# Optimization experiments

Measured on AMD Instinct MI355X. Metric: run time of the kernel, lower is better.

The kernel has to match this reference:

```python
import jax, jax.numpy as jnp
import numpy as np

N_NODES = 50000
N_EDGES = 800000
NODE_DIM = 128
EDGE_DIM = 16
HIDDEN = 64


def _gcn_conv(x, W, b, src, dst, n_nodes):
    """PyG-style GCNConv: add self-loops, symmetric deg^-1/2 normalization,
    aggregate messages from src into dst, then add bias. x: [N, Fin]."""
    h = x @ W  # [N, Fout]
    loops = jnp.arange(n_nodes)
    s = jnp.concatenate([src, loops])  # sources incl. self-loops
    d = jnp.concatenate([dst, loops])  # targets incl. self-loops
    deg = jax.ops.segment_sum(jnp.ones_like(d, dtype=h.dtype), d, num_segments=n_nodes)
    dinv = jax.lax.rsqrt(jnp.maximum(deg, 1.0))  # deg >= 1 thanks to self-loops
    norm = dinv[s] * dinv[d]  # [E+N]
    msg = h[s] * norm[:, None]  # gather + scale
    out = jax.ops.segment_sum(msg, d, num_segments=n_nodes)  # scatter-add
    return out + b


def setup_inputs() -> dict:
    key = jax.random.key(0)
    ks = jax.random.split(key, 12)
    x = jax.random.normal(ks[0], (N_NODES, NODE_DIM), dtype=jnp.float32)
    edge_index = jax.random.randint(ks[1], (2, N_EDGES), 0, N_NODES, dtype=jnp.int64)
    edge_attr = jax.random.normal(ks[2], (N_EDGES, EDGE_DIM), dtype=jnp.float32)
    def glorot(k, fan_in, fan_out):
        s = float(np.sqrt(2.0 / (fan_in + fan_out)))
        return jax.random.normal(k, (fan_in, fan_out), dtype=jnp.float32) * s
    W1 = glorot(ks[3], NODE_DIM, HIDDEN)
    b1 = jnp.zeros((HIDDEN,), jnp.float32)
    W2 = glorot(ks[4], HIDDEN, HIDDEN)
    b2 = jnp.zeros((HIDDEN,), jnp.float32)
    Wm1 = glorot(ks[5], 2 * HIDDEN + EDGE_DIM, HIDDEN)
    bm1 = jnp.zeros((HIDDEN,), jnp.float32)
    Wm2 = glorot(ks[6], HIDDEN, 2)
    bm2 = jnp.zeros((2,), jnp.float32)
    return {"x": x, "edge_index": edge_index, "edge_attr": edge_attr,
            "W1": W1, "b1": b1, "W2": W2, "b2": b2,
            "Wm1": Wm1, "bm1": bm1, "Wm2": Wm2, "bm2": bm2}


def reference(x, edge_index, edge_attr, W1, b1, W2, b2, Wm1, bm1, Wm2, bm2):
    n = x.shape[0]
    src, dst = edge_index[0], edge_index[1]
    h = jax.nn.relu(_gcn_conv(x, W1, b1, src, dst, n))
    h = jax.nn.relu(_gcn_conv(h, W2, b2, src, dst, n))
    # gather endpoint embeddings + concat edge features -> edge MLP
    edge_embed = jnp.concatenate([h[src], h[dst], edge_attr], axis=1)  # [E, 2H+Fe]
    out = jax.nn.relu(edge_embed @ Wm1 + bm1) @ Wm2 + bm2  # [E, 2]
    return out
```

## Files before the change

### kernel.cpp

```cpp
#include <hip/hip_runtime.h>
#include <hip/hip_fp16.h>


typedef float v4f __attribute__((ext_vector_type(4)));
typedef _Float16 v4h __attribute__((ext_vector_type(4)));

__device__ __forceinline__ float4 relu4(float4 v) {
    v.x = fmaxf(v.x, 0.f); v.y = fmaxf(v.y, 0.f);
    v.z = fmaxf(v.z, 0.f); v.w = fmaxf(v.w, 0.f);
    return v;
}

__device__ __forceinline__ void load_lds16(const void* g, void* l) {
    __builtin_amdgcn_global_load_lds(
        (const __attribute__((address_space(1))) void*)g,
        (__attribute__((address_space(3))) void*)l, 16, 0, 0);
}

__global__ void k_count(const int* __restrict__ dst, int* __restrict__ cnt,
                        int* __restrict__ rank, int E) {
    int e = blockIdx.x * 256 + threadIdx.x;
    if (e < E) rank[e] = atomicAdd(&cnt[dst[e]], 1);
}

__global__ void k_bsum(const int* __restrict__ cnt, int* __restrict__ bsum,
                       float* __restrict__ dinv, int N) {
    int i = blockIdx.x * 256 + threadIdx.x;
    int v = (i < N) ? cnt[i] : 0;
    if (i < N) dinv[i] = rsqrtf((float)v + 1.0f);
    int r = v;
#pragma unroll
    for (int d = 1; d < 64; d <<= 1) r += __shfl_xor(r, d);
    __shared__ int ws[4];
    if ((threadIdx.x & 63) == 0) ws[threadIdx.x >> 6] = r;
    __syncthreads();
    if (threadIdx.x == 0) bsum[blockIdx.x] = ws[0] + ws[1] + ws[2] + ws[3];
}

__global__ void k_scanb(int* __restrict__ bsum, int nb) {
    int t = threadIdx.x;
    int lane = t & 63, w = t >> 6;
    int v = (t < nb) ? bsum[t] : 0;
    int x = v;
#pragma unroll
    for (int d = 1; d < 64; d <<= 1) {
        int y = __shfl_up(x, d);
        if (lane >= d) x += y;
    }
    __shared__ int ws[4];
    if (lane == 63) ws[w] = x;
    __syncthreads();
    int woff = 0;
    for (int j = 0; j < w; j++) woff += ws[j];
    if (t < nb) bsum[t] = woff + x - v;
}

__global__ void k_scan3(const int* __restrict__ cnt, const int* __restrict__ bsum,
                        int* __restrict__ row_ptr, int N, int E) {
    int t = threadIdx.x, b = blockIdx.x;
    int i = b * 256 + t;
    int lane = t & 63, w = t >> 6;
    int v = (i < N) ? cnt[i] : 0;
    int x = v;
#pragma unroll
    for (int d = 1; d < 64; d <<= 1) {
        int y = __shfl_up(x, d);
        if (lane >= d) x += y;
    }
    __shared__ int ws[4];
    if (lane == 63) ws[w] = x;
    __syncthreads();
    int woff = 0;
    for (int j = 0; j < w; j++) woff += ws[j];
    if (i < N) row_ptr[i] = bsum[b] + woff + x - v;
    if (i == 0) row_ptr[N] = E;
}

__global__ void k_fill(const int* __restrict__ src, const int* __restrict__ dst,
                       const int* __restrict__ row_ptr, const int* __restrict__ rank,
                       int* __restrict__ csr_src, int E) {
    int e = blockIdx.x * 256 + threadIdx.x;
    if (e >= E) return;
    csr_src[row_ptr[dst[e]] + rank[e]] = src[e];
}

template<int K, bool RELU_A, bool SCALE, int NB>
__global__ __launch_bounds__(256) void k_mgemm(
    const float* __restrict__ A, const float* __restrict__ B0,
    const float* __restrict__ B1, const float* __restrict__ bias,
    const float* __restrict__ dinv, __half* __restrict__ C0,
    __half* __restrict__ C1, int M) {
    constexpr int P = K + 8;
    __shared__ __half As[64 * P];
    __shared__ __half Bs[NB * 64 * P];
    const int t = threadIdx.x;
    const int r0 = blockIdx.x * 64;

    constexpr int C4 = K / 4;
    for (int idx = t; idx < 64 * C4; idx += 256) {
        int row = idx / C4, c4 = idx % C4;
        float4 v = make_float4(0.f, 0.f, 0.f, 0.f);
        if (r0 + row < M)
            v = reinterpret_cast<const float4*>(A + (size_t)(r0 + row) * K)[c4];
        if (RELU_A) v = relu4(v);
        __half* d = &As[row * P + 4 * c4];
        d[0] = __float2half(v.x); d[1] = __float2half(v.y);
        d[2] = __float2half(v.z); d[3] = __float2half(v.w);
    }
    for (int m = 0; m < NB; m++) {
        const float* Bm = m ? B1 : B0;
        __half* Bsm = &Bs[m * 64 * P];
        for (int idx = t; idx < K * 16; idx += 256) {
            int k = idx >> 4, c4 = idx & 15;
            float4 v = reinterpret_cast<const float4*>(Bm + (size_t)k * 64)[c4];
            Bsm[(4 * c4 + 0) * P + k] = __float2half(v.x);
            Bsm[(4 * c4 + 1) * P + k] = __float2half(v.y);
            Bsm[(4 * c4 + 2) * P + k] = __float2half(v.z);
            Bsm[(4 * c4 + 3) * P + k] = __float2half(v.w);
        }
    }
    __syncthreads();

    const int lane = t & 63, w = t >> 6;
    const int li = lane & 15, g = lane >> 4;

    v4f acc[NB][4];
    const v4f zero = {0.f, 0.f, 0.f, 0.f};
#pragma unroll
    for (int m = 0; m < NB; m++)
#pragma unroll
        for (int c = 0; c < 4; c++) acc[m][c] = zero;

#pragma unroll
    for (int kk = 0; kk < K; kk += 16) {
        v4h a = *reinterpret_cast<const v4h*>(&As[(16 * w + li) * P + kk + 4 * g]);
#pragma unroll
        for (int m = 0; m < NB; m++) {
#pragma unroll
            for (int c = 0; c < 4; c++) {
                v4h b = *reinterpret_cast<const v4h*>(
                    &Bs[m * 64 * P + (16 * c + li) * P + kk + 4 * g]);
                acc[m][c] =
                    __builtin_amdgcn_mfma_f32_16x16x16f16(a, b, acc[m][c], 0, 0, 0);
            }
        }
    }

    const int rbase = r0 + 16 * w + 4 * g;
    float4 dv = make_float4(1.f, 1.f, 1.f, 1.f);
    if (SCALE) dv = *reinterpret_cast<const float4*>(&dinv[rbase]);
    const float sc[4] = {dv.x, dv.y, dv.z, dv.w};
#pragma unroll
    for (int m = 0; m < NB; m++) {
        __half* C = m ? C1 : C0;
#pragma unroll
        for (int c = 0; c < 4; c++) {
            int col = 16 * c + li;
            float badd = (NB == 2 && m == 0) ? bias[col] : 0.f;
#pragma unroll
            for (int r = 0; r < 4; r++) {
                int gr = rbase + r;
                if (gr < M)
                    C[(size_t)gr * 64 + col] =
                        __float2half(acc[m][c][r] * sc[r] + badd);
            }
        }
    }
}

__global__ __launch_bounds__(256, 4) void k_agg(const __half* __restrict__ A16,
                                                const int* __restrict__ row_ptr,
                                                const int* __restrict__ csr_src,
                                                const float* __restrict__ dinv,
                                                const float* __restrict__ bias,
                                                float* __restrict__ out, int N) {
    int gw = (blockIdx.x * 256 + threadIdx.x) >> 6;
    int sub = (threadIdx.x >> 4) & 3;
    int l = threadIdx.x & 15;
    int node = gw * 4 + sub;
    if (node >= N) return;
    const uint2* A4 = reinterpret_cast<const uint2*>(A16);

    int beg = row_ptr[node], end = row_ptr[node + 1];
    uint2 selfv = A4[(size_t)node * 16 + l];
    float2 a0 = __half22float2(*reinterpret_cast<__half2*>(&selfv.x));
    float2 a1 = __half22float2(*reinterpret_cast<__half2*>(&selfv.y));
    float4 acc = make_float4(a0.x, a0.y, a1.x, a1.y);

#define ACC(u)                                                          \
    {                                                                   \
        float2 f0 = __half22float2(*reinterpret_cast<__half2*>(&u.x));  \
        float2 f1 = __half22float2(*reinterpret_cast<__half2*>(&u.y));  \
        acc.x += f0.x; acc.y += f0.y; acc.z += f1.x; acc.w += f1.y;     \
    }
    for (int p = beg; p < end; p += 16) {
        int m = min(16, end - p);
        int sl = (p + l < end) ? csr_src[p + l] : 0;
        int j = 0;
        for (; j + 7 < m; j += 8) {
            uint2 u0 = A4[(size_t)__shfl(sl, j + 0, 16) * 16 + l];
            uint2 u1 = A4[(size_t)__shfl(sl, j + 1, 16) * 16 + l];
            uint2 u2 = A4[(size_t)__shfl(sl, j + 2, 16) * 16 + l];
            uint2 u3 = A4[(size_t)__shfl(sl, j + 3, 16) * 16 + l];
            uint2 u4 = A4[(size_t)__shfl(sl, j + 4, 16) * 16 + l];
            uint2 u5 = A4[(size_t)__shfl(sl, j + 5, 16) * 16 + l];
            uint2 u6 = A4[(size_t)__shfl(sl, j + 6, 16) * 16 + l];
            uint2 u7 = A4[(size_t)__shfl(sl, j + 7, 16) * 16 + l];
            ACC(u0) ACC(u1) ACC(u2) ACC(u3) ACC(u4) ACC(u5) ACC(u6) ACC(u7)
        }
        for (; j + 3 < m; j += 4) {
            uint2 u0 = A4[(size_t)__shfl(sl, j + 0, 16) * 16 + l];
            uint2 u1 = A4[(size_t)__shfl(sl, j + 1, 16) * 16 + l];
            uint2 u2 = A4[(size_t)__shfl(sl, j + 2, 16) * 16 + l];
            uint2 u3 = A4[(size_t)__shfl(sl, j + 3, 16) * 16 + l];
            ACC(u0) ACC(u1) ACC(u2) ACC(u3)
        }
        for (; j < m; j++) {
            uint2 u0 = A4[(size_t)__shfl(sl, j, 16) * 16 + l];
            ACC(u0)
        }
    }
#undef ACC
    float di = dinv[node];
    float4 bb = *reinterpret_cast<const float4*>(&bias[4 * l]);
    float4 o = make_float4(fmaf(di, acc.x, bb.x), fmaf(di, acc.y, bb.y),
                           fmaf(di, acc.z, bb.z), fmaf(di, acc.w, bb.w));
    *reinterpret_cast<float4*>(&out[(size_t)node * 64 + 4 * l]) = o;
}

__global__ __launch_bounds__(256, 4) void k_edge(
    const __half* __restrict__ Ps, const __half* __restrict__ Pd,
    const int* __restrict__ src, const int* __restrict__ dst,
    const float* __restrict__ ea, const float* __restrict__ We,
    const float* __restrict__ Wm2, const float* __restrict__ bm2,
    float* __restrict__ out, int E) {
    __shared__ __align__(16) char smem[4 * 12288];
    const int lane = threadIdx.x & 63;
    const int wid = (blockIdx.x * 256 + threadIdx.x) >> 6;
    const int li = lane & 15, g = lane >> 4;
    const int e0 = wid * 64;
    if (e0 >= E) return;

    char* wbase = smem + (threadIdx.x >> 6) * 12288;
    const float4* ea4 = reinterpret_cast<const float4*>(ea);

    v4h af[4];
#pragma unroll
    for (int m = 0; m < 4; m++) {
        v4h a;
#pragma unroll
        for (int i = 0; i < 4; i++)
            a[i] = (_Float16)We[(4 * g + i) * 64 + 16 * m + li];
        af[m] = a;
    }

    float4 w2lo[4], w2hi[4];
#pragma unroll
    for (int m = 0; m < 4; m++) {
        int dim0 = 16 * m + 4 * g;
        w2lo[m] = *reinterpret_cast<const float4*>(&Wm2[2 * dim0]);
        w2hi[m] = *reinterpret_cast<const float4*>(&Wm2[2 * dim0 + 4]);
    }
    const float c0 = bm2[0], c1 = bm2[1];

    const int ecl = min(e0 + lane, E - 1);
    const int sv = src[ecl], dv = dst[ecl];

    v4h bh[4];
#pragma unroll
    for (int n = 0; n < 4; n++) {
        int ee = min(e0 + 16 * n + li, E - 1);
        float4 bf = ea4[(size_t)ee * 4 + g];
        v4h t;
        t[0] = (_Float16)bf.x; t[1] = (_Float16)bf.y;
        t[2] = (_Float16)bf.z; t[3] = (_Float16)bf.w;
        bh[n] = t;
    }

    const int jrow = lane >> 3;
    const int csw = (lane & 7) ^ jrow;

#define STAGE(n, b)                                                              \
    {                                                                            \
        char* lb = wbase + (b) * 4096 + lane * 16;                               \
        int n0 = __shfl(sv, 16 * (n) + jrow);                                    \
        int n1 = __shfl(sv, 16 * (n) + 8 + jrow);                                \
        int n2 = __shfl(dv, 16 * (n) + jrow);                                    \
        int n3 = __shfl(dv, 16 * (n) + 8 + jrow);                                \
        load_lds16((const char*)Ps + (size_t)n0 * 128 + (csw << 4), lb);         \
        load_lds16((const char*)Ps + (size_t)n1 * 128 + (csw << 4), lb + 1024);  \
        load_lds16((const char*)Pd + (size_t)n2 * 128 + (csw << 4), lb + 2048);  \
        load_lds16((const char*)Pd + (size_t)n3 * 128 + (csw << 4), lb + 3072);  \
    }

    float p0s[4], p1s[4];

#define COMPUTE(n, b)                                                             \
    {                                                                             \
        const char* rb = wbase + (b) * 4096;                                      \
        uint2 us[4], ud[4];                                                       \
        _Pragma("unroll")                                                         \
        for (int m = 0; m < 4; m++) {                                             \
            int q = 4 * m + g;                                                    \
            int off = li * 128 + ((((q >> 1) ^ (li & 7)) << 4) | ((q & 1) << 3)); \
            us[m] = *reinterpret_cast<const uint2*>(rb + off);                    \
            ud[m] = *reinterpret_cast<const uint2*>(rb + 2048 + off);             \
        }                                                                         \
        float p0_ = 0.f, p1_ = 0.f;                                               \
        _Pragma("unroll")                                                         \
        for (int m = 0; m < 4; m++) {                                             \
            float2 s0 = __half22float2(*reinterpret_cast<__half2*>(&us[m].x));    \
            float2 s1 = __half22float2(*reinterpret_cast<__half2*>(&us[m].y));    \
            float2 d0 = __half22float2(*reinterpret_cast<__half2*>(&ud[m].x));    \
            float2 d1 = __half22float2(*reinterpret_cast<__half2*>(&ud[m].y));    \
            v4f c;                                                                \
            c[0] = s0.x + d0.x;                                                   \
            c[1] = s0.y + d0.y;                                                   \
            c[2] = s1.x + d1.x;                                                   \
            c[3] = s1.y + d1.y;                                                   \
            v4f q = __builtin_amdgcn_mfma_f32_16x16x16f16(af[m], bh[n], c, 0, 0, 0); \
            float u0 = fmaxf(q[0], 0.f), u1 = fmaxf(q[1], 0.f);                   \
            float u2 = fmaxf(q[2], 0.f), u3 = fmaxf(q[3], 0.f);                   \
            p0_ += u0 * w2lo[m].x + u1 * w2lo[m].z + u2 * w2hi[m].x + u3 * w2hi[m].z; \
            p1_ += u0 * w2lo[m].y + u1 * w2lo[m].w + u2 * w2hi[m].y + u3 * w2hi[m].w; \
        }                                                                         \
        p0_ += __shfl_xor(p0_, 16); p0_ += __shfl_xor(p0_, 32);                   \
        p1_ += __shfl_xor(p1_, 16); p1_ += __shfl_xor(p1_, 32);                   \
        p0s[n] = p0_; p1s[n] = p1_;                                               \
    }

    STAGE(0, 0)
    STAGE(1, 1)
    STAGE(2, 2)
    asm volatile("s_waitcnt vmcnt(8)" ::: "memory");
    COMPUTE(0, 0)
    STAGE(3, 0)
    asm volatile("s_waitcnt vmcnt(8)" ::: "memory");
    COMPUTE(1, 1)
    asm volatile("s_waitcnt vmcnt(4)" ::: "memory");
    COMPUTE(2, 2)
    asm volatile("s_waitcnt vmcnt(0)" ::: "memory");
    COMPUTE(3, 0)
#undef STAGE
#undef COMPUTE

    if (g == 0) {
#pragma unroll
        for (int n = 0; n < 4; n++) {
            int e = e0 + 16 * n + li;
            if (e < E)
                *reinterpret_cast<float2*>(&out[(size_t)e * 2]) =
                    make_float2(p0s[n] + c0, p1s[n] + c1);
        }
    }
}

static inline size_t align256(size_t x) { return (x + 255) & ~(size_t)255; }

extern "C" void kernel_launch(void* const* d_in, const int* in_sizes, int n_in,
                              void* d_out, int out_size, void* d_ws, size_t ws_size,
                              hipStream_t stream) {
    const float* x = (const float*)d_in[0];
    const int* ei = (const int*)d_in[1];
    const float* ea = (const float*)d_in[2];
    const float* W1 = (const float*)d_in[3];
    const float* b1 = (const float*)d_in[4];
    const float* W2 = (const float*)d_in[5];
    const float* b2 = (const float*)d_in[6];
    const float* Wm1 = (const float*)d_in[7];
    const float* bm1 = (const float*)d_in[8];
    const float* Wm2 = (const float*)d_in[9];
    const float* bm2 = (const float*)d_in[10];

    const int N = in_sizes[0] / 128;
    const int E = in_sizes[1] / 2;
    const int* src = ei;
    const int* dst = ei + E;
    float* out = (float*)d_out;

    const int NB = (N + 255) / 256;

    char* p = (char*)d_ws;
    int* cnt = (int*)p;        p += align256((size_t)N * 4);
    int* rank = (int*)p;       p += align256((size_t)E * 4);
    int* row_ptr = (int*)p;    p += align256((size_t)(N + 1) * 4);
    int* bsum = (int*)p;       p += align256((size_t)NB * 4);
    int* csr_src = (int*)p;    p += align256((size_t)E * 4);
    float* dinv = (float*)p;   p += align256((size_t)N * 4);
    __half* A16 = (__half*)p;  p += align256((size_t)N * 64 * 2);
    float* B = (float*)p;      p += align256((size_t)N * 64 * 4);
    __half* Ps16 = (__half*)p; p += align256((size_t)N * 64 * 2);
    __half* Pd16 = (__half*)p;

    hipMemsetAsync(cnt, 0, (size_t)N * sizeof(int), stream);
    k_count<<<(E + 255) / 256, 256, 0, stream>>>(dst, cnt, rank, E);
    k_bsum<<<NB, 256, 0, stream>>>(cnt, bsum, dinv, N);
    k_scanb<<<1, 256, 0, stream>>>(bsum, NB);
    k_scan3<<<NB, 256, 0, stream>>>(cnt, bsum, row_ptr, N, E);
    k_fill<<<(E + 255) / 256, 256, 0, stream>>>(src, dst, row_ptr, rank, csr_src, E);

    const int GB = (N + 63) / 64;

    k_mgemm<128, false, true, 1><<<GB, 256, 0, stream>>>(
        x, W1, nullptr, nullptr, dinv, A16, nullptr, N);
    k_agg<<<(N + 15) / 16, 256, 0, stream>>>(A16, row_ptr, csr_src, dinv, b1, B, N);

    k_mgemm<64, true, true, 1><<<GB, 256, 0, stream>>>(
        B, W2, nullptr, nullptr, dinv, A16, nullptr, N);
    k_agg<<<(N + 15) / 16, 256, 0, stream>>>(A16, row_ptr, csr_src, dinv, b2, B, N);

    k_mgemm<64, true, false, 2><<<GB, 256, 0, stream>>>(
        B, Wm1, Wm1 + 64 * 64, bm1, nullptr, Ps16, Pd16, N);
    int waves = (E + 63) / 64;
    k_edge<<<(waves + 3) / 4, 256, 0, stream>>>(Ps16, Pd16, src, dst, ea,
                                                Wm1 + 128 * 64, Wm2, bm2,
                                                out, E);
}
```

Before: 276.4 us.

## Fuse neighbor aggregation with the following GEMM via shared-memory tiles

Merges each GCN aggregation kernel with the next dense matmul. The aggregated, ReLU'd rows are written as fp16 into shared memory and fed directly to MFMA instead of going through a float32 global buffer. This removes the fp32 intermediate round trip and two kernel launches. In exchange, each block now runs the irregular gather before its GEMM, and occupancy is no longer governed by the separate launch bounds, so latency hiding for the gathers may change.

```diff
diff --git a/kernel.cpp b/kernel.cpp
--- a/kernel.cpp
+++ b/kernel.cpp
@@ -84,15 +84,13 @@
     csr_src[row_ptr[dst[e]] + rank[e]] = src[e];
 }
 
-template<int K, bool RELU_A, bool SCALE, int NB>
+template<int K, bool RELU_A, bool SCALE>
 __global__ __launch_bounds__(256) void k_mgemm(
     const float* __restrict__ A, const float* __restrict__ B0,
-    const float* __restrict__ B1, const float* __restrict__ bias,
-    const float* __restrict__ dinv, __half* __restrict__ C0,
-    __half* __restrict__ C1, int M) {
+    const float* __restrict__ dinv, __half* __restrict__ C0, int M) {
     constexpr int P = K + 8;
     __shared__ __half As[64 * P];
-    __shared__ __half Bs[NB * 64 * P];
+    __shared__ __half Bs[64 * P];
     const int t = threadIdx.x;
     const int r0 = blockIdx.x * 64;
 
@@ -107,10 +105,73 @@
         d[0] = __float2half(v.x); d[1] = __float2half(v.y);
         d[2] = __float2half(v.z); d[3] = __float2half(v.w);
     }
+    for (int idx = t; idx < K * 16; idx += 256) {
+        int k = idx >> 4, c4 = idx & 15;
+        float4 v = reinterpret_cast<const float4*>(B0 + (size_t)k * 64)[c4];
+        Bs[(4 * c4 + 0) * P + k] = __float2half(v.x);
+        Bs[(4 * c4 + 1) * P + k] = __float2half(v.y);
+        Bs[(4 * c4 + 2) * P + k] = __float2half(v.z);
+        Bs[(4 * c4 + 3) * P + k] = __float2half(v.w);
+    }
+    __syncthreads();
+
+    const int lane = t & 63, w = t >> 6;
+    const int li = lane & 15, g = lane >> 4;
+
+    v4f acc[4];
+    const v4f zero = {0.f, 0.f, 0.f, 0.f};
+#pragma unroll
+    for (int c = 0; c < 4; c++) acc[c] = zero;
+
+#pragma unroll
+    for (int kk = 0; kk < K; kk += 16) {
+        v4h a = *reinterpret_cast<const v4h*>(&As[(16 * w + li) * P + kk + 4 * g]);
+#pragma unroll
+        for (int c = 0; c < 4; c++) {
+            v4h b = *reinterpret_cast<const v4h*>(&Bs[(16 * c + li) * P + kk + 4 * g]);
+            acc[c] = __builtin_amdgcn_mfma_f32_16x16x16f16(a, b, acc[c], 0, 0, 0);
+        }
+    }
+
+    const int rbase = r0 + 16 * w + 4 * g;
+    float4 dv = make_float4(1.f, 1.f, 1.f, 1.f);
+    if (SCALE && rbase + 3 < M) dv = *reinterpret_cast<const float4*>(&dinv[rbase]);
+    else if (SCALE) {
+        dv.x = (rbase < M) ? dinv[rbase] : 1.f;
+        dv.y = (rbase + 1 < M) ? dinv[rbase + 1] : 1.f;
+        dv.z = (rbase + 2 < M) ? dinv[rbase + 2] : 1.f;
+        dv.w = (rbase + 3 < M) ? dinv[rbase + 3] : 1.f;
+    }
+    const float sc[4] = {dv.x, dv.y, dv.z, dv.w};
+#pragma unroll
+    for (int c = 0; c < 4; c++) {
+        int col = 16 * c + li;
+#pragma unroll
+        for (int r = 0; r < 4; r++) {
+            int gr = rbase + r;
+            if (gr < M)
+                C0[(size_t)gr * 64 + col] = __float2half(acc[c][r] * sc[r]);
+        }
+    }
+}
+
+template<int NB, bool SCALE_OUT>
+__global__ __launch_bounds__(256) void k_aggemm(
+    const __half* __restrict__ Ain, const int* __restrict__ row_ptr,
+    const int* __restrict__ csr_src, const float* __restrict__ dinv,
+    const float* __restrict__ bias_agg, const float* __restrict__ B0,
+    const float* __restrict__ B1, const float* __restrict__ bias_out,
+    __half* __restrict__ C0, __half* __restrict__ C1, int N) {
+    constexpr int P = 72;
+    __shared__ __half As[64 * P];
+    __shared__ __half Bs[NB * 64 * P];
+    const int t = threadIdx.x;
+    const int r0 = blockIdx.x * 64;
+
     for (int m = 0; m < NB; m++) {
         const float* Bm = m ? B1 : B0;
         __half* Bsm = &Bs[m * 64 * P];
-        for (int idx = t; idx < K * 16; idx += 256) {
+        for (int idx = t; idx < 64 * 16; idx += 256) {
             int k = idx >> 4, c4 = idx & 15;
             float4 v = reinterpret_cast<const float4*>(Bm + (size_t)k * 64)[c4];
             Bsm[(4 * c4 + 0) * P + k] = __float2half(v.x);
@@ -119,6 +180,69 @@
             Bsm[(4 * c4 + 3) * P + k] = __float2half(v.w);
         }
     }
+
+    const uint2* A4 = reinterpret_cast<const uint2*>(Ain);
+    const int l = t & 15;
+    const int grp = t >> 4;
+    const float4 bb = *reinterpret_cast<const float4*>(&bias_agg[4 * l]);
+
+#define ACC(u)                                                          \
+    {                                                                   \
+        float2 f0 = __half22float2(*reinterpret_cast<__half2*>(&u.x));  \
+        float2 f1 = __half22float2(*reinterpret_cast<__half2*>(&u.y));  \
+        acc.x += f0.x; acc.y += f0.y; acc.z += f1.x; acc.w += f1.y;     \
+    }
+    for (int c = 0; c < 4; c++) {
+        int nl = c * 16 + grp;
+        int node = r0 + nl;
+        float4 ov = make_float4(0.f, 0.f, 0.f, 0.f);
+        if (node < N) {
+            int beg = row_ptr[node], end = row_ptr[node + 1];
+            uint2 selfv = A4[(size_t)node * 16 + l];
+            float2 a0 = __half22float2(*reinterpret_cast<__half2*>(&selfv.x));
+            float2 a1 = __half22float2(*reinterpret_cast<__half2*>(&selfv.y));
+            float4 acc = make_float4(a0.x, a0.y, a1.x, a1.y);
+            for (int p = beg; p < end; p += 16) {
+                int m = min(16, end - p);
+                int sl = (p + l < end) ? csr_src[p + l] : 0;
+                int j = 0;
+                for (; j + 7 < m; j += 8) {
+                    uint2 u0 = A4[(size_t)__shfl(sl, j + 0, 16) * 16 + l];
+                    uint2 u1 = A4[(size_t)__shfl(sl, j + 1, 16) * 16 + l];
+                    uint2 u2 = A4[(size_t)__shfl(sl, j + 2, 16) * 16 + l];
+                    uint2 u3 = A4[(size_t)__shfl(sl, j + 3, 16) * 16 + l];
+                    uint2 u4 = A4[(size_t)__shfl(sl, j + 4, 16) * 16 + l];
+                    uint2 u5 = A4[(size_t)__shfl(sl, j + 5, 16) * 16 + l];
+                    uint2 u6 = A4[(size_t)__shfl(sl, j + 6, 16) * 16 + l];
+                    uint2 u7 = A4[(size_t)__shfl(sl, j + 7, 16) * 16 + l];
+                    ACC(u0) ACC(u1) ACC(u2) ACC(u3) ACC(u4) ACC(u5) ACC(u6) ACC(u7)
+                }
+                for (; j + 3 < m; j += 4) {
+                    uint2 u0 = A4[(size_t)__shfl(sl, j + 0, 16) * 16 + l];
+                    uint2 u1 = A4[(size_t)__shfl(sl, j + 1, 16) * 16 + l];
+                    uint2 u2 = A4[(size_t)__shfl(sl, j + 2, 16) * 16 + l];
+                    uint2 u3 = A4[(size_t)__shfl(sl, j + 3, 16) * 16 + l];
+                    ACC(u0) ACC(u1) ACC(u2) ACC(u3)
+                }
+                for (; j < m; j++) {
+                    uint2 u0 = A4[(size_t)__shfl(sl, j, 16) * 16 + l];
+                    ACC(u0)
+                }
+            }
+            float di = dinv[node];
+            ov.x = fmaxf(fmaf(di, acc.x, bb.x), 0.f);
+            ov.y = fmaxf(fmaf(di, acc.y, bb.y), 0.f);
+            ov.z = fmaxf(fmaf(di, acc.z, bb.z), 0.f);
+            ov.w = fmaxf(fmaf(di, acc.w, bb.w), 0.f);
+        }
+        __half2 lo = __floats2half2_rn(ov.x, ov.y);
+        __half2 hi = __floats2half2_rn(ov.z, ov.w);
+        uint2 raw;
+        raw.x = *reinterpret_cast<unsigned*>(&lo);
+        raw.y = *reinterpret_cast<unsigned*>(&hi);
+        *reinterpret_cast<uint2*>(&As[nl * P + 4 * l]) = raw;
+    }
+#undef ACC
     __syncthreads();
 
     const int lane = t & 63, w = t >> 6;
@@ -132,7 +256,7 @@
         for (int c = 0; c < 4; c++) acc[m][c] = zero;
 
 #pragma unroll
-    for (int kk = 0; kk < K; kk += 16) {
+    for (int kk = 0; kk < 64; kk += 16) {
         v4h a = *reinterpret_cast<const v4h*>(&As[(16 * w + li) * P + kk + 4 * g]);
 #pragma unroll
         for (int m = 0; m < NB; m++) {
@@ -147,85 +271,28 @@
     }
 
     const int rbase = r0 + 16 * w + 4 * g;
-    float4 dv = make_float4(1.f, 1.f, 1.f, 1.f);
-    if (SCALE) dv = *reinterpret_cast<const float4*>(&dinv[rbase]);
-    const float sc[4] = {dv.x, dv.y, dv.z, dv.w};
+    float sc[4] = {1.f, 1.f, 1.f, 1.f};
+    if (SCALE_OUT) {
+#pragma unroll
+        for (int r = 0; r < 4; r++)
+            sc[r] = (rbase + r < N) ? dinv[rbase + r] : 1.f;
+    }
 #pragma unroll
     for (int m = 0; m < NB; m++) {
         __half* C = m ? C1 : C0;
 #pragma unroll
         for (int c = 0; c < 4; c++) {
             int col = 16 * c + li;
-            float badd = (NB == 2 && m == 0) ? bias[col] : 0.f;
+            float badd = (NB == 2 && m == 0) ? bias_out[col] : 0.f;
 #pragma unroll
             for (int r = 0; r < 4; r++) {
                 int gr = rbase + r;
-                if (gr < M)
+                if (gr < N)
                     C[(size_t)gr * 64 + col] =
                         __float2half(acc[m][c][r] * sc[r] + badd);
             }
         }
     }
-}
-
-__global__ __launch_bounds__(256, 4) void k_agg(const __half* __restrict__ A16,
-                                                const int* __restrict__ row_ptr,
-                                                const int* __restrict__ csr_src,
-                                                const float* __restrict__ dinv,
-                                                const float* __restrict__ bias,
-                                                float* __restrict__ out, int N) {
-    int gw = (blockIdx.x * 256 + threadIdx.x) >> 6;
-    int sub = (threadIdx.x >> 4) & 3;
-    int l = threadIdx.x & 15;
-    int node = gw * 4 + sub;
-    if (node >= N) return;
-    const uint2* A4 = reinterpret_cast<const uint2*>(A16);
-
-    int beg = row_ptr[node], end = row_ptr[node + 1];
-    uint2 selfv = A4[(size_t)node * 16 + l];
-    float2 a0 = __half22float2(*reinterpret_cast<__half2*>(&selfv.x));
-    float2 a1 = __half22float2(*reinterpret_cast<__half2*>(&selfv.y));
-    float4 acc = make_float4(a0.x, a0.y, a1.x, a1.y);
-
-#define ACC(u)                                                          \
-    {                                                                   \
-        float2 f0 = __half22float2(*reinterpret_cast<__half2*>(&u.x));  \
-        float2 f1 = __half22float2(*reinterpret_cast<__half2*>(&u.y));  \
-        acc.x += f0.x; acc.y += f0.y; acc.z += f1.x; acc.w += f1.y;     \
-    }
-    for (int p = beg; p < end; p += 16) {
-        int m = min(16, end - p);
-        int sl = (p + l < end) ? csr_src[p + l] : 0;
-        int j = 0;
-        for (; j + 7 < m; j += 8) {
-            uint2 u0 = A4[(size_t)__shfl(sl, j + 0, 16) * 16 + l];
-            uint2 u1 = A4[(size_t)__shfl(sl, j + 1, 16) * 16 + l];
-            uint2 u2 = A4[(size_t)__shfl(sl, j + 2, 16) * 16 + l];
-            uint2 u3 = A4[(size_t)__shfl(sl, j + 3, 16) * 16 + l];
-            uint2 u4 = A4[(size_t)__shfl(sl, j + 4, 16) * 16 + l];
-            uint2 u5 = A4[(size_t)__shfl(sl, j + 5, 16) * 16 + l];
-            uint2 u6 = A4[(size_t)__shfl(sl, j + 6, 16) * 16 + l];
-            uint2 u7 = A4[(size_t)__shfl(sl, j + 7, 16) * 16 + l];
-            ACC(u0) ACC(u1) ACC(u2) ACC(u3) ACC(u4) ACC(u5) ACC(u6) ACC(u7)
-        }
-        for (; j + 3 < m; j += 4) {
-            uint2 u0 = A4[(size_t)__shfl(sl, j + 0, 16) * 16 + l];
-            uint2 u1 = A4[(size_t)__shfl(sl, j + 1, 16) * 16 + l];
-            uint2 u2 = A4[(size_t)__shfl(sl, j + 2, 16) * 16 + l];
-            uint2 u3 = A4[(size_t)__shfl(sl, j + 3, 16) * 16 + l];
-            ACC(u0) ACC(u1) ACC(u2) ACC(u3)
-        }
-        for (; j < m; j++) {
-            uint2 u0 = A4[(size_t)__shfl(sl, j, 16) * 16 + l];
-            ACC(u0)
-        }
-    }
-#undef ACC
-    float di = dinv[node];
-    float4 bb = *reinterpret_cast<const float4*>(&bias[4 * l]);
-    float4 o = make_float4(fmaf(di, acc.x, bb.x), fmaf(di, acc.y, bb.y),
-                           fmaf(di, acc.z, bb.z), fmaf(di, acc.w, bb.w));
-    *reinterpret_cast<float4*>(&out[(size_t)node * 64 + 4 * l]) = o;
 }
 
 __global__ __launch_bounds__(256, 4) void k_edge(
@@ -381,15 +448,15 @@
     const int NB = (N + 255) / 256;
 
     char* p = (char*)d_ws;
-    int* cnt = (int*)p;        p += align256((size_t)N * 4);
-    int* rank = (int*)p;       p += align256((size_t)E * 4);
-    int* row_ptr = (int*)p;    p += align256((size_t)(N + 1) * 4);
-    int* bsum = (int*)p;       p += align256((size_t)NB * 4);
-    int* csr_src = (int*)p;    p += align256((size_t)E * 4);
-    float* dinv = (float*)p;   p += align256((size_t)N * 4);
-    __half* A16 = (__half*)p;  p += align256((size_t)N * 64 * 2);
-    float* B = (float*)p;      p += align256((size_t)N * 64 * 4);
-    __half* Ps16 = (__half*)p; p += align256((size_t)N * 64 * 2);
+    int* cnt = (int*)p;         p += align256((size_t)N * 4);
+    int* rank = (int*)p;        p += align256((size_t)E * 4);
+    int* row_ptr = (int*)p;     p += align256((size_t)(N + 1) * 4);
+    int* bsum = (int*)p;        p += align256((size_t)NB * 4);
+    int* csr_src = (int*)p;     p += align256((size_t)E * 4);
+    float* dinv = (float*)p;    p += align256((size_t)N * 4);
+    __half* A16a = (__half*)p;  p += align256((size_t)N * 64 * 2);
+    __half* A16b = (__half*)p;  p += align256((size_t)N * 64 * 2);
+    __half* Ps16 = (__half*)p;  p += align256((size_t)N * 64 * 2);
     __half* Pd16 = (__half*)p;
 
     hipMemsetAsync(cnt, 0, (size_t)N * sizeof(int), stream);
@@ -401,16 +468,16 @@
 
     const int GB = (N + 63) / 64;
 
-    k_mgemm<128, false, true, 1><<<GB, 256, 0, stream>>>(
-        x, W1, nullptr, nullptr, dinv, A16, nullptr, N);
-    k_agg<<<(N + 15) / 16, 256, 0, stream>>>(A16, row_ptr, csr_src, dinv, b1, B, N);
-
-    k_mgemm<64, true, true, 1><<<GB, 256, 0, stream>>>(
-        B, W2, nullptr, nullptr, dinv, A16, nullptr, N);
-    k_agg<<<(N + 15) / 16, 256, 0, stream>>>(A16, row_ptr, csr_src, dinv, b2, B, N);
-
-    k_mgemm<64, true, false, 2><<<GB, 256, 0, stream>>>(
-        B, Wm1, Wm1 + 64 * 64, bm1, nullptr, Ps16, Pd16, N);
+    k_mgemm<128, false, true><<<GB, 256, 0, stream>>>(x, W1, dinv, A16a, N);
+
+    k_aggemm<1, true><<<GB, 256, 0, stream>>>(
+        A16a, row_ptr, csr_src, dinv, b1, W2, nullptr, nullptr,
+        A16b, nullptr, N);
+
+    k_aggemm<2, false><<<GB, 256, 0, stream>>>(
+        A16b, row_ptr, csr_src, dinv, b2, Wm1, Wm1 + 64 * 64, bm1,
+        Ps16, Pd16, N);
+
     int waves = (E + 63) / 64;
     k_edge<<<(waves + 3) / 4, 256, 0, stream>>>(Ps16, Pd16, src, dst, ea,
                                                 Wm1 + 128 * 64, Wm2, bm2,
```

New measurement: 282.7 us. +2.3%, slower.
